# Kernel tuning notes

Measured on AMD Instinct MI355X. Metric: run time of the kernel, lower is better.

## Reference

```python
import jax, jax.numpy as jnp
import numpy as np

SCALE = 1.0 / np.sqrt(512.0).astype(np.float32)  # attention() hardcodes d_k=512


def setup_inputs() -> dict:
    key = jax.random.key(0)
    ks = jax.random.split(key, 9)
    B, S, D = 4, 2048, 512
    mk = lambda k, shape: jax.random.normal(k, shape, dtype=jnp.float32) * 0.05
    return {
        "q": mk(ks[0], (B, S, D)),
        "k": mk(ks[1], (B, S, D)),
        "v": mk(ks[2], (B, S, D)),
        "WQ_w": mk(ks[3], (D, D)),
        "WQ_b": mk(ks[4], (D,)),
        "WK_w": mk(ks[5], (D, D)),
        "WK_b": mk(ks[6], (D,)),
        "WV_w": mk(ks[7], (D, D)),
        "WV_b": mk(ks[8], (D,)),
    }


def reference(q, k, v, WQ_w, WQ_b, WK_w, WK_b, WV_w, WV_b):
    # torch nn.Linear: y = x @ W.T + b
    qp = q @ WQ_w.T + WQ_b  # [B,S,dk]
    kp = k @ WK_w.T + WK_b  # [B,S,dk]
    vp = v @ WV_w.T + WV_b  # [B,S,dv]
    qk = jnp.einsum("bqd,bkd->bqk", qp, kp) * SCALE  # [B,Sq,Sk]
    S = qk.shape[1]
    tril = jnp.tril(jnp.ones((S, S), dtype=qk.dtype))  # multiplicative causal mask
    qk = qk * tril
    # NOTE: original applies softmax over dim=1 (the query axis), faithfully kept.
    attn = jax.nn.softmax(qk, axis=1)
    out = jnp.einsum("bqk,bkd->bqd", attn, vp)  # [B,Sq,dv]
    return out
```

## Files before the change

### kernel.cpp

```cpp
#include <hip/hip_runtime.h>
#include <hip/hip_bf16.h>


#define S_LEN 2048
#define D_DIM 512
#define SCALE_F 0.044194173824159216f

typedef __attribute__((ext_vector_type(8))) short s8v;
typedef __attribute__((ext_vector_type(4))) short s4v;
typedef __attribute__((ext_vector_type(4))) float f4v;

enum { EPI_BIAS = 0, EPI_BIAS_T = 1, EPI_SCORES = 2 };

#define SBAR()    asm volatile("s_barrier" ::: "memory")
#define WAITV(n)  asm volatile("s_waitcnt vmcnt(" #n ")" ::: "memory")

__device__ __forceinline__ short f2bf_s(float f) {
  union { __hip_bfloat16 b; short s; } u; u.b = __float2bfloat16(f); return u.s;
}
__device__ __forceinline__ float bf2f_s(short h) {
  union { short s; __hip_bfloat16 b; } u; u.s = h; return __bfloat162float(u.b);
}

__device__ __forceinline__ void glds16(const short* g, short* l) {
  __builtin_amdgcn_global_load_lds((const __attribute__((address_space(1))) void*)g,
                                   (__attribute__((address_space(3))) void*)l, 16, 0, 0);
}

template <int EPI>
__device__ __forceinline__ void gemm_core(
    const short* __restrict__ A, const short* __restrict__ B,
    short* __restrict__ C, const float* __restrict__ bias,
    short* SMEM, int N, int K, size_t sCz, int m0, int n0, int bz,
    float* __restrict__ Z)
{
  const int tid  = threadIdx.x;
  const int w    = tid >> 6;
  const int lane = tid & 63;
  const int quad = lane >> 4;
  const int l16  = lane & 15;
  const int wm   = (w >> 1) * 64;
  const int wn   = (w & 1) * 64;

  const int strow = tid >> 3;
  const int gl = ((tid & 7) ^ (strow & 7)) * 8;

  f4v acc[4][4];
#pragma unroll
  for (int i = 0; i < 4; ++i)
#pragma unroll
    for (int j = 0; j < 4; ++j)
#pragma unroll
      for (int r = 0; r < 4; ++r) acc[i][j][r] = 0.0f;

  const short* Ag = A + (size_t)(m0 + strow) * K + gl;
  const short* Bg = B + (size_t)(n0 + strow) * K + gl;
  const size_t pstr = (size_t)32 * K;
  const int t8 = tid * 8;
  const int swq = l16 & 7;

  const int niter = K >> 6;

#pragma unroll
  for (int p = 0; p < 4; ++p) glds16(Ag + p * pstr, SMEM + t8 + p * 2048);
#pragma unroll
  for (int p = 0; p < 4; ++p) glds16(Bg + p * pstr, SMEM + 8192 + t8 + p * 2048);

  for (int i = 0; i < niter; ++i) {
    const int c = i & 1;
    if (i + 1 < niter) {
      const int k1 = (i + 1) << 6;
      short* dA = SMEM + (1 - c) * 16384 + t8;
#pragma unroll
      for (int p = 0; p < 4; ++p) glds16(Ag + k1 + p * pstr, dA + p * 2048);
#pragma unroll
      for (int p = 0; p < 4; ++p) glds16(Bg + k1 + p * pstr, dA + 8192 + p * 2048);
      WAITV(8);
    } else {
      WAITV(0);
    }
    SBAR();

    const short* As = SMEM + c * 16384;
    const short* Bs = As + 8192;
#pragma unroll
    for (int kk = 0; kk < 2; ++kk) {
      s8v af[4], bf[4];
#pragma unroll
      for (int ii = 0; ii < 4; ++ii)
        af[ii] = *(const s8v*)&As[(wm + ii * 16 + l16) * 64 + (((kk * 4 + quad) ^ swq) * 8)];
#pragma unroll
      for (int j = 0; j < 4; ++j)
        bf[j] = *(const s8v*)&Bs[(wn + j * 16 + l16) * 64 + (((kk * 4 + quad) ^ swq) * 8)];
#pragma unroll
      for (int ii = 0; ii < 4; ++ii)
#pragma unroll
        for (int j = 0; j < 4; ++j)
          acc[ii][j] = __builtin_amdgcn_mfma_f32_16x16x32_bf16(af[ii], bf[j], acc[ii][j], 0, 0, 0);
    }
    SBAR();
  }

  float bv[4];
  if (EPI == EPI_BIAS || EPI == EPI_BIAS_T) {
#pragma unroll
    for (int j = 0; j < 4; ++j) bv[j] = bias[n0 + wn + j * 16 + l16];
  }

  if (EPI == EPI_BIAS_T) {
#pragma unroll
    for (int i = 0; i < 4; ++i) {
#pragma unroll
      for (int j = 0; j < 4; ++j) {
        const int gn  = n0 + wn + j * 16 + l16;
        const int gmb = m0 + wm + i * 16 + quad * 4;
        const int bb = gmb >> 11, ssb = gmb & (S_LEN - 1);
        s4v o;
#pragma unroll
        for (int r = 0; r < 4; ++r) o[r] = f2bf_s(acc[i][j][r] + bv[j]);
        *(s4v*)&C[((size_t)bb * D_DIM + gn) * S_LEN + ssb] = o;
      }
    }
    return;
  }

  short* TB = SMEM;
  const int wbase = w * 2176;
  float csum[4] = {0.f, 0.f, 0.f, 0.f};

#pragma unroll
  for (int ph = 0; ph < 2; ++ph) {
    __syncthreads();
#pragma unroll
    for (int ii = 0; ii < 2; ++ii) {
      const int i = ph * 2 + ii;
#pragma unroll
      for (int j = 0; j < 4; ++j) {
        const int gn = n0 + wn + j * 16 + l16;
#pragma unroll
        for (int r = 0; r < 4; ++r) {
          short o;
          if (EPI == EPI_SCORES) {
            const int gm = m0 + wm + i * 16 + quad * 4 + r;
            const float f = (gm >= gn) ? (__expf(acc[i][j][r] * SCALE_F) - 1.0f) : 0.0f;
            csum[j] += f;
            o = f2bf_s(f);
          } else {
            o = f2bf_s(acc[i][j][r] + bv[j]);
          }
          TB[wbase + (ii * 16 + quad * 4 + r) * 68 + j * 16 + l16] = o;
        }
      }
    }
    __syncthreads();
#pragma unroll
    for (int p = 0; p < 4; ++p) {
      const int row = p * 8 + (lane >> 3);
      const int cg  = lane & 7;
      const s8v vv = *(const s8v*)&TB[wbase + row * 68 + cg * 8];
      const int gm = m0 + wm + ph * 32 + row;
      const int gn = n0 + wn + cg * 8;
      *(s8v*)&C[sCz + (size_t)gm * N + gn] = vv;
    }
  }

  if (EPI == EPI_SCORES) {
#pragma unroll
    for (int j = 0; j < 4; ++j) {
      float cs = csum[j];
      cs += __shfl_xor(cs, 16, 64);
      cs += __shfl_xor(cs, 32, 64);
      if (quad == 0) atomicAdd(&Z[(bz << 11) + n0 + wn + j * 16 + l16], cs);
    }
  }
}

__global__ __launch_bounds__(256, 2) void gemm_scoresF(
    const short* __restrict__ A, const short* __restrict__ B, short* __restrict__ C,
    float* __restrict__ Z)
{
  __shared__ __align__(16) short SMEM[32768];
  const int bz = blockIdx.z;
  const int t = blockIdx.x;
  int ti = (int)((sqrtf(8.0f * t + 1.0f) - 1.0f) * 0.5f);
  while ((ti + 1) * (ti + 2) / 2 <= t) ++ti;
  while (ti * (ti + 1) / 2 > t) --ti;
  const int tj = t - ti * (ti + 1) / 2;
  gemm_core<EPI_SCORES>(A + (size_t)bz * S_LEN * D_DIM, B + (size_t)bz * S_LEN * D_DIM,
                        C, nullptr, SMEM, S_LEN, D_DIM,
                        (size_t)bz * S_LEN * S_LEN, ti * 128, tj * 128, bz, Z);
}

__global__ __launch_bounds__(256, 2) void proj3(
    const short* __restrict__ a0, const short* __restrict__ a1, const short* __restrict__ a2,
    const short* __restrict__ b0, const short* __restrict__ b1, const short* __restrict__ b2,
    short* __restrict__ c0, short* __restrict__ c1, short* __restrict__ c2,
    const float* __restrict__ x0, const float* __restrict__ x1, const float* __restrict__ x2)
{
  __shared__ __align__(16) short SMEM[32768];
  const int z = blockIdx.z;
  const short* A = (z == 0) ? a0 : (z == 1) ? a1 : a2;
  const short* B = (z == 0) ? b0 : (z == 1) ? b1 : b2;
  short*       C = (z == 0) ? c0 : (z == 1) ? c1 : c2;
  const float* bias = (z == 0) ? x0 : (z == 1) ? x1 : x2;
  if (z == 2)
    gemm_core<EPI_BIAS_T>(A, B, C, bias, SMEM, D_DIM, D_DIM, 0,
                          blockIdx.y * 128, blockIdx.x * 128, 0, nullptr);
  else
    gemm_core<EPI_BIAS>(A, B, C, bias, SMEM, D_DIM, D_DIM, 0,
                        blockIdx.y * 128, blockIdx.x * 128, 0, nullptr);
}

__global__ __launch_bounds__(256, 2) void gemm_outF(
    const short* __restrict__ F, const short* __restrict__ vpT,
    const float* __restrict__ Tv, float* __restrict__ out)
{
  __shared__ __align__(16) short SMEM[36864];

  const int tid  = threadIdx.x;
  const int bz   = blockIdx.z;
  const int m0   = (31 - blockIdx.y) * 64;
  const int n0   = blockIdx.x * 128;

  const short* A = F   + (size_t)bz * S_LEN * S_LEN;
  const short* B = vpT + (size_t)bz * D_DIM * S_LEN;

  const int w    = tid >> 6;
  const int lane = tid & 63;
  const int quad = lane >> 4;
  const int l16  = lane & 15;
  const int wm   = (w >> 1) * 32;
  const int wn   = (w & 1) * 64;

  const int strow = tid >> 3;
  const int gl = ((tid & 7) ^ (strow & 7)) * 8;

  f4v acc[2][4];
#pragma unroll
  for (int i = 0; i < 2; ++i)
#pragma unroll
    for (int j = 0; j < 4; ++j)
#pragma unroll
      for (int r = 0; r < 4; ++r) acc[i][j][r] = 0.0f;

  const short* Ag = A + (size_t)(m0 + strow) * S_LEN + gl;
  const short* Bg = B + (size_t)(n0 + strow) * S_LEN + gl;
  const size_t pstr = (size_t)32 * S_LEN;
  const int t8 = tid * 8;
  const int swq = l16 & 7;

  const int niter = (m0 >> 6) + 1;

#pragma unroll
  for (int pre = 0; pre < 2; ++pre) {
    short* dst = SMEM + pre * 12288 + t8;
    const int k0 = pre << 6;
#pragma unroll
    for (int p = 0; p < 2; ++p) glds16(Ag + k0 + p * pstr, dst + p * 2048);
#pragma unroll
    for (int p = 0; p < 4; ++p) glds16(Bg + k0 + p * pstr, dst + 4096 + p * 2048);
  }

  int cbuf = 0, nbuf = 2;
  for (int i = 0; i < niter; ++i) {
    if (i + 2 < niter) {
      const int k2 = (i + 2) << 6;
      short* dst = SMEM + nbuf * 12288 + t8;
#pragma unroll
      for (int p = 0; p < 2; ++p) glds16(Ag + k2 + p * pstr, dst + p * 2048);
#pragma unroll
      for (int p = 0; p < 4; ++p) glds16(Bg + k2 + p * pstr, dst + 4096 + p * 2048);
      nbuf = (nbuf == 2) ? 0 : nbuf + 1;
      WAITV(12);
    } else if (i + 1 < niter) {
      WAITV(6);
    } else {
      WAITV(0);
    }
    SBAR();

    const short* As = SMEM + cbuf * 12288;
    const short* Bs = As + 4096;
    cbuf = (cbuf == 2) ? 0 : cbuf + 1;
#pragma unroll
    for (int kk = 0; kk < 2; ++kk) {
      s8v af[2], bf[4];
#pragma unroll
      for (int ii = 0; ii < 2; ++ii)
        af[ii] = *(const s8v*)&As[(wm + ii * 16 + l16) * 64 + (((kk * 4 + quad) ^ swq) * 8)];
#pragma unroll
      for (int j = 0; j < 4; ++j)
        bf[j] = *(const s8v*)&Bs[(wn + j * 16 + l16) * 64 + (((kk * 4 + quad) ^ swq) * 8)];
#pragma unroll
      for (int ii = 0; ii < 2; ++ii)
#pragma unroll
        for (int j = 0; j < 4; ++j)
          acc[ii][j] = __builtin_amdgcn_mfma_f32_16x16x32_bf16(af[ii], bf[j], acc[ii][j], 0, 0, 0);
    }
    SBAR();
  }

  float* Cf = out + (size_t)bz * S_LEN * D_DIM;
#pragma unroll
  for (int i = 0; i < 2; ++i) {
#pragma unroll
    for (int j = 0; j < 4; ++j) {
      const int gn = n0 + wn + j * 16 + l16;
      const float tvn = Tv[(bz << 9) + gn];
#pragma unroll
      for (int r = 0; r < 4; ++r) {
        const int gm = m0 + wm + i * 16 + quad * 4 + r;
        Cf[(size_t)gm * D_DIM + gn] = acc[i][j][r] + tvn;
      }
    }
  }
}

__global__ __launch_bounds__(256) void cvt3(
    const float* __restrict__ s0, const float* __restrict__ s1,
    const float* __restrict__ s2, short* __restrict__ dst, int n)
{
  const float* s = (blockIdx.y == 0) ? s0 : (blockIdx.y == 1) ? s1 : s2;
  short* d = dst + (size_t)blockIdx.y * n;
  const int i = (blockIdx.x * 256 + threadIdx.x) * 8;
  if (i >= n) return;
  const float4 f0 = *(const float4*)(s + i);
  const float4 f1 = *(const float4*)(s + i + 4);
  s8v o;
  o[0] = f2bf_s(f0.x); o[1] = f2bf_s(f0.y); o[2] = f2bf_s(f0.z); o[3] = f2bf_s(f0.w);
  o[4] = f2bf_s(f1.x); o[5] = f2bf_s(f1.y); o[6] = f2bf_s(f1.z); o[7] = f2bf_s(f1.w);
  *(s8v*)(d + i) = o;
}

__global__ __launch_bounds__(256) void scale_vpt_T(
    short* __restrict__ vpT, const float* __restrict__ ZF, float* __restrict__ Tv)
{
  __shared__ float red[4];
  const int b = blockIdx.y, d = blockIdx.x, tid = threadIdx.x;
  const size_t rowbase = ((size_t)(b * D_DIM + d)) * S_LEN;
  const float* zf = ZF + (b << 11);
  const int k0 = tid * 8;

  s8v v = *(s8v*)&vpT[rowbase + k0];
  float s = 0.0f;
#pragma unroll
  for (int i = 0; i < 8; ++i) {
    const float w = bf2f_s(v[i]) / (2048.0f + zf[k0 + i]);
    s += w;
    v[i] = f2bf_s(w);
  }
  *(s8v*)&vpT[rowbase + k0] = v;

#pragma unroll
  for (int off = 32; off >= 1; off >>= 1) s += __shfl_xor(s, off, 64);
  if ((tid & 63) == 0) red[tid >> 6] = s;
  __syncthreads();
  if (tid == 0) Tv[(b << 9) + d] = red[0] + red[1] + red[2] + red[3];
}

extern "C" void kernel_launch(void* const* d_in, const int* in_sizes, int n_in,
                              void* d_out, int out_size, void* d_ws, size_t ws_size,
                              hipStream_t stream) {
  const float* q   = (const float*)d_in[0];
  const float* k   = (const float*)d_in[1];
  const float* v   = (const float*)d_in[2];
  const float* WQw = (const float*)d_in[3];
  const float* WQb = (const float*)d_in[4];
  const float* WKw = (const float*)d_in[5];
  const float* WKb = (const float*)d_in[6];
  const float* WVw = (const float*)d_in[7];
  const float* WVb = (const float*)d_in[8];

  char* ws = (char*)d_ws;
  short* F   = (short*)(ws);
  short* qb  = (short*)(ws);
  short* Wqb = (short*)(ws + 25165824);
  short* qp  = (short*)(ws + 33554432);
  short* kp  = (short*)(ws + 41943040);
  short* vpT = (short*)(ws + 50331648);
  float* ZF  = (float*)(ws + 58720256);
  float* Tv  = (float*)(ws + 58753024);
  short* kb  = qb + 4194304;
  short* vb  = qb + 8388608;
  short* Wkb = Wqb + 262144;
  short* Wvb = Wqb + 524288;

  const dim3 blk(256);

  hipMemsetAsync(ZF, 0, 4 * S_LEN * sizeof(float), stream);

  cvt3<<<dim3(2048, 3), blk, 0, stream>>>(q, k, v, qb, 4194304);
  cvt3<<<dim3(128, 3), blk, 0, stream>>>(WQw, WKw, WVw, Wqb, 262144);

  proj3<<<dim3(4, 64, 3), blk, 0, stream>>>(
      qb, kb, vb, Wqb, Wkb, Wvb, qp, kp, vpT, WQb, WKb, WVb);

  gemm_scoresF<<<dim3(136, 1, 4), blk, 0, stream>>>(qp, kp, F, ZF);

  scale_vpt_T<<<dim3(512, 4), blk, 0, stream>>>(vpT, ZF, Tv);

  gemm_outF<<<dim3(4, 32, 4), blk, 0, stream>>>(F, vpT, Tv, (float*)d_out);
}
```

Measured before the change: 183.6 us.

## Tune GEMM scheduling, XCD block swizzle, fuse conversions, reorder outF pipeline

Replaces the LDS fragment loads with inline ds_read_b128 on precomputed addresses, adds sched barriers and s_setprio around the MFMA bursts, and moves the outF prefetch after the barrier so each iteration needs only one barrier. The scores, projection and output kernels are flattened to 1D grids with an XCD-aware block swizzle, and outF interleaves long and short causal rows to balance load. The two conversion launches are merged into one. These aim to cut launch overhead, scheduling stalls and tail imbalance, at the cost of compiler-opaque asm that forces an lgkmcnt(0) wait before every MFMA burst.

```diff
diff --git a/kernel.cpp b/kernel.cpp
--- a/kernel.cpp
+++ b/kernel.cpp
@@ -12,8 +12,10 @@
 
 enum { EPI_BIAS = 0, EPI_BIAS_T = 1, EPI_SCORES = 2 };
 
-#define SBAR()    asm volatile("s_barrier" ::: "memory")
-#define WAITV(n)  asm volatile("s_waitcnt vmcnt(" #n ")" ::: "memory")
+#define SBAR()    __builtin_amdgcn_s_barrier()
+#define SCHEDB()  __builtin_amdgcn_sched_barrier(0)
+#define WAITV(n)  asm volatile("s_waitcnt vmcnt(" #n ")")
+#define WAITL0()  asm volatile("s_waitcnt lgkmcnt(0)")
 
 __device__ __forceinline__ short f2bf_s(float f) {
   union { __hip_bfloat16 b; short s; } u; u.b = __float2bfloat16(f); return u.s;
@@ -25,6 +27,16 @@
 __device__ __forceinline__ void glds16(const short* g, short* l) {
   __builtin_amdgcn_global_load_lds((const __attribute__((address_space(1))) void*)g,
                                    (__attribute__((address_space(3))) void*)l, 16, 0, 0);
+}
+
+__device__ __forceinline__ unsigned lds_addr(const short* p) {
+  return (unsigned)(unsigned long long)(const __attribute__((address_space(3))) short*)p;
+}
+
+__device__ __forceinline__ s8v dsr128(unsigned a) {
+  s8v r;
+  asm volatile("ds_read_b128 %0, %1" : "=&v"(r) : "v"(a));
+  return r;
 }
 
 template <int EPI>
@@ -59,6 +71,15 @@
   const int t8 = tid * 8;
   const int swq = l16 & 7;
 
+  const unsigned base = lds_addr(SMEM);
+  unsigned aoff[4], boff[4];
+#pragma unroll
+  for (int ii = 0; ii < 4; ++ii)
+    aoff[ii] = base + (unsigned)((wm + ii * 16 + l16) * 128 + ((quad ^ swq) * 16));
+#pragma unroll
+  for (int j = 0; j < 4; ++j)
+    boff[j] = base + 16384u + (unsigned)((wn + j * 16 + l16) * 128 + ((quad ^ swq) * 16));
+
   const int niter = K >> 6;
 
 #pragma unroll
@@ -75,28 +96,32 @@
       for (int p = 0; p < 4; ++p) glds16(Ag + k1 + p * pstr, dA + p * 2048);
 #pragma unroll
       for (int p = 0; p < 4; ++p) glds16(Bg + k1 + p * pstr, dA + 8192 + p * 2048);
+      SCHEDB();
       WAITV(8);
     } else {
       WAITV(0);
     }
     SBAR();
-
-    const short* As = SMEM + c * 16384;
-    const short* Bs = As + 8192;
+    SCHEDB();
+
+    const unsigned cofs = (unsigned)(c << 15);
 #pragma unroll
     for (int kk = 0; kk < 2; ++kk) {
+      const unsigned kx = (unsigned)(kk << 6);
       s8v af[4], bf[4];
 #pragma unroll
-      for (int ii = 0; ii < 4; ++ii)
-        af[ii] = *(const s8v*)&As[(wm + ii * 16 + l16) * 64 + (((kk * 4 + quad) ^ swq) * 8)];
-#pragma unroll
-      for (int j = 0; j < 4; ++j)
-        bf[j] = *(const s8v*)&Bs[(wn + j * 16 + l16) * 64 + (((kk * 4 + quad) ^ swq) * 8)];
+      for (int ii = 0; ii < 4; ++ii) af[ii] = dsr128((aoff[ii] ^ kx) + cofs);
+#pragma unroll
+      for (int j = 0; j < 4; ++j)   bf[j]  = dsr128((boff[j] ^ kx) + cofs);
+      WAITL0();
+      SCHEDB();
+      __builtin_amdgcn_s_setprio(1);
 #pragma unroll
       for (int ii = 0; ii < 4; ++ii)
 #pragma unroll
         for (int j = 0; j < 4; ++j)
           acc[ii][j] = __builtin_amdgcn_mfma_f32_16x16x32_bf16(af[ii], bf[j], acc[ii][j], 0, 0, 0);
+      __builtin_amdgcn_s_setprio(0);
     }
     SBAR();
   }
@@ -180,8 +205,10 @@
     float* __restrict__ Z)
 {
   __shared__ __align__(16) short SMEM[32768];
-  const int bz = blockIdx.z;
-  const int t = blockIdx.x;
+  const int bid = blockIdx.x;
+  const int bsw = (bid & 7) * 68 + (bid >> 3);
+  const int bz  = bsw / 136;
+  const int t   = bsw - bz * 136;
   int ti = (int)((sqrtf(8.0f * t + 1.0f) - 1.0f) * 0.5f);
   while ((ti + 1) * (ti + 2) / 2 <= t) ++ti;
   while (ti * (ti + 1) / 2 > t) --ti;
@@ -198,17 +225,20 @@
     const float* __restrict__ x0, const float* __restrict__ x1, const float* __restrict__ x2)
 {
   __shared__ __align__(16) short SMEM[32768];
-  const int z = blockIdx.z;
+  const int bid = blockIdx.x;
+  const int bsw = (bid & 7) * 96 + (bid >> 3);
+  const int z   = bsw >> 8;
+  const int rem = bsw & 255;
+  const int m0  = (rem >> 2) * 128;
+  const int n0  = (rem & 3) * 128;
   const short* A = (z == 0) ? a0 : (z == 1) ? a1 : a2;
   const short* B = (z == 0) ? b0 : (z == 1) ? b1 : b2;
   short*       C = (z == 0) ? c0 : (z == 1) ? c1 : c2;
   const float* bias = (z == 0) ? x0 : (z == 1) ? x1 : x2;
   if (z == 2)
-    gemm_core<EPI_BIAS_T>(A, B, C, bias, SMEM, D_DIM, D_DIM, 0,
-                          blockIdx.y * 128, blockIdx.x * 128, 0, nullptr);
+    gemm_core<EPI_BIAS_T>(A, B, C, bias, SMEM, D_DIM, D_DIM, 0, m0, n0, 0, nullptr);
   else
-    gemm_core<EPI_BIAS>(A, B, C, bias, SMEM, D_DIM, D_DIM, 0,
-                        blockIdx.y * 128, blockIdx.x * 128, 0, nullptr);
+    gemm_core<EPI_BIAS>(A, B, C, bias, SMEM, D_DIM, D_DIM, 0, m0, n0, 0, nullptr);
 }
 
 __global__ __launch_bounds__(256, 2) void gemm_outF(
@@ -218,9 +248,12 @@
   __shared__ __align__(16) short SMEM[36864];
 
   const int tid  = threadIdx.x;
-  const int bz   = blockIdx.z;
-  const int m0   = (31 - blockIdx.y) * 64;
-  const int n0   = blockIdx.x * 128;
+  const int h    = blockIdx.x;
+  const int n0   = (h & 3) * 128;
+  const int bz   = (h >> 2) & 3;
+  const int zs   = h >> 4;
+  const int mi   = (zs < 16) ? (31 - zs) : (zs - 16);
+  const int m0   = mi * 64;
 
   const short* A = F   + (size_t)bz * S_LEN * S_LEN;
   const short* B = vpT + (size_t)bz * D_DIM * S_LEN;
@@ -249,7 +282,16 @@
   const int t8 = tid * 8;
   const int swq = l16 & 7;
 
-  const int niter = (m0 >> 6) + 1;
+  const unsigned base = lds_addr(SMEM);
+  unsigned aoff[2], boff[4];
+#pragma unroll
+  for (int ii = 0; ii < 2; ++ii)
+    aoff[ii] = base + (unsigned)((wm + ii * 16 + l16) * 128 + ((quad ^ swq) * 16));
+#pragma unroll
+  for (int j = 0; j < 4; ++j)
+    boff[j] = base + 8192u + (unsigned)((wn + j * 16 + l16) * 128 + ((quad ^ swq) * 16));
+
+  const int niter = mi + 1;
 
 #pragma unroll
   for (int pre = 0; pre < 2; ++pre) {
@@ -261,43 +303,43 @@
     for (int p = 0; p < 4; ++p) glds16(Bg + k0 + p * pstr, dst + 4096 + p * 2048);
   }
 
-  int cbuf = 0, nbuf = 2;
+  int cbuf = 0;
   for (int i = 0; i < niter; ++i) {
+    if (i + 1 < niter) { WAITV(6); } else { WAITV(0); }
+    SBAR();
+    SCHEDB();
+
     if (i + 2 < niter) {
+      int nb = cbuf + 2; if (nb >= 3) nb -= 3;
       const int k2 = (i + 2) << 6;
-      short* dst = SMEM + nbuf * 12288 + t8;
+      short* dst = SMEM + nb * 12288 + t8;
 #pragma unroll
       for (int p = 0; p < 2; ++p) glds16(Ag + k2 + p * pstr, dst + p * 2048);
 #pragma unroll
       for (int p = 0; p < 4; ++p) glds16(Bg + k2 + p * pstr, dst + 4096 + p * 2048);
-      nbuf = (nbuf == 2) ? 0 : nbuf + 1;
-      WAITV(12);
-    } else if (i + 1 < niter) {
-      WAITV(6);
-    } else {
-      WAITV(0);
-    }
-    SBAR();
-
-    const short* As = SMEM + cbuf * 12288;
-    const short* Bs = As + 4096;
+      SCHEDB();
+    }
+
+    const unsigned cofs = (unsigned)(cbuf * 24576);
     cbuf = (cbuf == 2) ? 0 : cbuf + 1;
 #pragma unroll
     for (int kk = 0; kk < 2; ++kk) {
+      const unsigned kx = (unsigned)(kk << 6);
       s8v af[2], bf[4];
 #pragma unroll
-      for (int ii = 0; ii < 2; ++ii)
-        af[ii] = *(const s8v*)&As[(wm + ii * 16 + l16) * 64 + (((kk * 4 + quad) ^ swq) * 8)];
-#pragma unroll
-      for (int j = 0; j < 4; ++j)
-        bf[j] = *(const s8v*)&Bs[(wn + j * 16 + l16) * 64 + (((kk * 4 + quad) ^ swq) * 8)];
+      for (int ii = 0; ii < 2; ++ii) af[ii] = dsr128((aoff[ii] ^ kx) + cofs);
+#pragma unroll
+      for (int j = 0; j < 4; ++j)   bf[j]  = dsr128((boff[j] ^ kx) + cofs);
+      WAITL0();
+      SCHEDB();
+      __builtin_amdgcn_s_setprio(1);
 #pragma unroll
       for (int ii = 0; ii < 2; ++ii)
 #pragma unroll
         for (int j = 0; j < 4; ++j)
           acc[ii][j] = __builtin_amdgcn_mfma_f32_16x16x32_bf16(af[ii], bf[j], acc[ii][j], 0, 0, 0);
-    }
-    SBAR();
+      __builtin_amdgcn_s_setprio(0);
+    }
   }
 
   float* Cf = out + (size_t)bz * S_LEN * D_DIM;
@@ -316,14 +358,22 @@
   }
 }
 
-__global__ __launch_bounds__(256) void cvt3(
-    const float* __restrict__ s0, const float* __restrict__ s1,
-    const float* __restrict__ s2, short* __restrict__ dst, int n)
-{
-  const float* s = (blockIdx.y == 0) ? s0 : (blockIdx.y == 1) ? s1 : s2;
-  short* d = dst + (size_t)blockIdx.y * n;
-  const int i = (blockIdx.x * 256 + threadIdx.x) * 8;
-  if (i >= n) return;
+__global__ __launch_bounds__(256) void cvt_all(
+    const float* __restrict__ q, const float* __restrict__ k, const float* __restrict__ v,
+    const float* __restrict__ wq, const float* __restrict__ wk, const float* __restrict__ wv,
+    short* __restrict__ qb, short* __restrict__ Wqb)
+{
+  const int y = blockIdx.y;
+  const float* s; short* d; int i;
+  if (blockIdx.x < 2048) {
+    s = (y == 0) ? q : (y == 1) ? k : v;
+    d = qb + (size_t)y * 4194304;
+    i = (blockIdx.x * 256 + threadIdx.x) * 8;
+  } else {
+    s = (y == 0) ? wq : (y == 1) ? wk : wv;
+    d = Wqb + (size_t)y * 262144;
+    i = ((int)(blockIdx.x - 2048) * 256 + threadIdx.x) * 8;
+  }
   const float4 f0 = *(const float4*)(s + i);
   const float4 f1 = *(const float4*)(s + i + 4);
   s8v o;
@@ -387,17 +437,16 @@
 
   const dim3 blk(256);
 
-  hipMemsetAsync(ZF, 0, 4 * S_LEN * sizeof(float), stream);
-
-  cvt3<<<dim3(2048, 3), blk, 0, stream>>>(q, k, v, qb, 4194304);
-  cvt3<<<dim3(128, 3), blk, 0, stream>>>(WQw, WKw, WVw, Wqb, 262144);
-
-  proj3<<<dim3(4, 64, 3), blk, 0, stream>>>(
+  (void)hipMemsetAsync(ZF, 0, 4 * S_LEN * sizeof(float), stream);
+
+  cvt_all<<<dim3(2176, 3), blk, 0, stream>>>(q, k, v, WQw, WKw, WVw, qb, Wqb);
+
+  proj3<<<dim3(768), blk, 0, stream>>>(
       qb, kb, vb, Wqb, Wkb, Wvb, qp, kp, vpT, WQb, WKb, WVb);
 
-  gemm_scoresF<<<dim3(136, 1, 4), blk, 0, stream>>>(qp, kp, F, ZF);
+  gemm_scoresF<<<dim3(544), blk, 0, stream>>>(qp, kp, F, ZF);
 
   scale_vpt_T<<<dim3(512, 4), blk, 0, stream>>>(vpT, ZF, Tv);
 
-  gemm_outF<<<dim3(4, 32, 4), blk, 0, stream>>>(F, vpT, Tv, (float*)d_out);
-}
+  gemm_outF<<<dim3(512), blk, 0, stream>>>(F, vpT, Tv, (float*)d_out);
+}
```

Measured after the change: 168.5 us. -8.2%, faster.
